# Kernel tuning notes

Hardware: AMD Instinct MI355X
Metric: run time of the kernel (lower is better)

Reference implementation:

```python
import jax, jax.numpy as jnp
import numpy as np

EPS = 1e-08   # clip eps from __init__
M = 0.2       # angular margin
B, D, C = 512, 512, 100000


def setup_inputs() -> dict:
    key = jax.random.key(0)
    k1, k2, k3 = jax.random.split(key, 3)
    x = jax.random.normal(k1, (B, D), dtype=jnp.float32)
    weight = jax.random.normal(k2, (C, D), dtype=jnp.float32)
    y = jax.random.randint(k3, (B,), 0, C, dtype=jnp.int64)
    rescale = jnp.ones((1,), dtype=jnp.float32)
    return {"x": x, "y": y, "weight": weight, "rescale": rescale}


def _l2norm(v, axis=-1, eps=1e-12):
    # matches F.normalize(p=2): v / max(||v||, eps)
    n = jnp.sqrt(jnp.sum(v * v, axis=axis, keepdims=True))
    return v / jnp.maximum(n, eps)


def reference(x, y, weight, rescale):
    # cos similarities: [B, C]
    fc = jnp.clip(_l2norm(x) @ _l2norm(weight).T, -1.0 + EPS, 1.0 - EPS)
    fc_w_margin = jnp.cos(jnp.arccos(fc) + M)
    # inject margin only at the target class (one-hot where-select)
    is_target = jax.nn.one_hot(y, C, dtype=jnp.bool_)
    logit = jnp.where(is_target, fc_w_margin, fc)
    # faithful to original: softmax, then CrossEntropyLoss on the probs
    res = jax.nn.softmax(rescale * logit, axis=-1)
    logp = jax.nn.log_softmax(res, axis=-1)
    nll = -jnp.take_along_axis(logp, y[:, None], axis=1)[:, 0]
    return jnp.mean(nll)
```

## Files before the change

### kernel.cpp

```cpp
#include <hip/hip_runtime.h>
#include <math.h>

#define BB 512
#define DD 512
#define CC 100000
#define CCPAD 100096
#define MARGIN 0.2f
#define CLIP_EPS 1e-8f
#define NCOLT 782

typedef float f32x4  __attribute__((ext_vector_type(4)));

#define XN8_BYTES   262144u
#define P_BYTES     1601536u
#define PBASE       XN8_BYTES
#define AUX_OFF     (PBASE + 3u * P_BYTES)

__device__ inline unsigned f2e4m3(float a) {
    unsigned u = __builtin_bit_cast(unsigned, a);
    unsigned s = (u >> 24) & 0x80u;
    float ab = fabsf(a);
    unsigned code;
    if (ab >= 0.015625f) {
        unsigned r = (u & 0x7FFFFFFFu) + 0x7FFFFu + ((u >> 20) & 1u);
        int e = (int)(r >> 23) - 127;
        unsigned m = (r >> 20) & 7u;
        code = (unsigned)((e + 7) << 3) | m;
    } else {
        code = (unsigned)rintf(ab * 512.0f);
    }
    return s | code;
}

__device__ inline int soff8(int row, int b) {
    return row * 64 + ((((b >> 4) ^ ((row >> 1) & 3)) << 4)) + (b & 15);
}

__global__ __launch_bounds__(256) void k_norm_x(const float* __restrict__ x,
                                                unsigned char* __restrict__ XN8,
                                                float* __restrict__ out) {
    int row = blockIdx.x, tid = threadIdx.x;
    float2 v = *(const float2*)(x + row * DD + tid * 2);
    float ss = v.x * v.x + v.y * v.y;
    for (int m = 1; m < 64; m <<= 1) ss += __shfl_xor(ss, m, 64);
    __shared__ float sm[4];
    int wid = tid >> 6, lane = tid & 63;
    if (lane == 0) sm[wid] = ss;
    __syncthreads();
    float inv = 1.0f / fmaxf(sqrtf(sm[0] + sm[1] + sm[2] + sm[3]), 1e-12f);
    unsigned c0 = f2e4m3(v.x * inv), c1 = f2e4m3(v.y * inv);
    *(unsigned short*)(XN8 + row * DD + tid * 2) = (unsigned short)(c0 | (c1 << 8));
    if (row == 0 && tid == 0) out[0] = 0.0f;
}

__global__ __launch_bounds__(256) void k_wnormc(const float* __restrict__ w,
                                                unsigned char* __restrict__ WN8) {
    int wid = threadIdx.x >> 6, lane = threadIdx.x & 63;
    int row = blockIdx.x * 4 + wid;
    unsigned* o0 = (unsigned*)(WN8 + (size_t)row * DD + 4 * lane);
    unsigned* o1 = (unsigned*)(WN8 + (size_t)row * DD + 256 + 4 * lane);
    if (row >= CC) { *o0 = 0u; *o1 = 0u; return; }
    const float4* wr = (const float4*)(w + (size_t)row * DD);
    float4 a = wr[lane];
    float4 b = wr[lane + 64];
    float ss = a.x*a.x + a.y*a.y + a.z*a.z + a.w*a.w
             + b.x*b.x + b.y*b.y + b.z*b.z + b.w*b.w;
    for (int m = 1; m < 64; m <<= 1) ss += __shfl_xor(ss, m, 64);
    float inv = 1.0f / fmaxf(sqrtf(ss), 1e-12f);
    *o0 = f2e4m3(a.x*inv) | (f2e4m3(a.y*inv) << 8) | (f2e4m3(a.z*inv) << 16) | (f2e4m3(a.w*inv) << 24);
    *o1 = f2e4m3(b.x*inv) | (f2e4m3(b.y*inv) << 8) | (f2e4m3(b.z*inv) << 16) | (f2e4m3(b.w*inv) << 24);
}

__global__ __launch_bounds__(256) void k_gemm8(const unsigned char* __restrict__ WN8,
                                               const unsigned char* __restrict__ XN8,
                                               const float* __restrict__ rescale_p,
                                               float* __restrict__ ZP,
                                               float* __restrict__ S2P,
                                               float* __restrict__ S3P) {
    __shared__ __align__(16) unsigned char Wt[3][128 * 64];
    __shared__ __align__(16) unsigned char Xs[3][128 * 64];
    __shared__ float st[2][2][64][3];

    int h = blockIdx.x;
    int logical = (h & 7) * 391 + (h >> 3);
    int ct = logical >> 2;
    int bt = logical & 3;

    int tid = threadIdx.x;
    int lane = tid & 63, wid = tid >> 6;
    int wr = wid >> 1, wc = wid & 1;
    float rescale = rescale_p[0];

    int rl0 = wid * 16 + (lane >> 2);
    int j0  = lane & 3;
    const unsigned char* wbase = WN8 + (size_t)(ct * 128) * DD;
    const unsigned char* xbase = XN8 + (size_t)(bt * 128) * DD;

    auto STAGE = [&](int b, int kt) {
#pragma unroll
        for (int i = 0; i < 2; ++i) {
            int rl = i * 64 + rl0;
            int jsrc = j0 ^ ((rl >> 1) & 3);
            const unsigned char* ws_ = wbase + (size_t)rl * DD + kt * 64 + jsrc * 16;
            const unsigned char* xs_ = xbase + (size_t)rl * DD + kt * 64 + jsrc * 16;
            unsigned char* wd = &Wt[b][(i * 256 + wid * 64) * 16];
            unsigned char* xd = &Xs[b][(i * 256 + wid * 64) * 16];
            __builtin_amdgcn_global_load_lds(
                (const __attribute__((address_space(1))) void*)ws_,
                (__attribute__((address_space(3))) void*)wd, 16, 0, 0);
            __builtin_amdgcn_global_load_lds(
                (const __attribute__((address_space(1))) void*)xs_,
                (__attribute__((address_space(3))) void*)xd, 16, 0, 0);
        }
    };

    int roA[2][4], roB[2][4];
#pragma unroll
    for (int sl = 0; sl < 2; ++sl)
#pragma unroll
        for (int i = 0; i < 4; ++i) {
            int bb = sl * 32 + (lane >> 4) * 8;
            roA[sl][i] = soff8(wr * 64 + i * 16 + (lane & 15), bb);
            roB[sl][i] = soff8(wc * 64 + i * 16 + (lane & 15), bb);
        }

    f32x4 acc[4][4];
#pragma unroll
    for (int i = 0; i < 4; i++)
#pragma unroll
        for (int j = 0; j < 4; j++) acc[i][j] = (f32x4){0.f, 0.f, 0.f, 0.f};

    auto COMPUTE = [&](int b) {
#pragma unroll
        for (int sl = 0; sl < 2; ++sl) {
            long a[4], bb[4];
#pragma unroll
            for (int i = 0; i < 4; i++) a[i]  = *(const long*)&Wt[b][roA[sl][i]];
#pragma unroll
            for (int i = 0; i < 4; i++) bb[i] = *(const long*)&Xs[b][roB[sl][i]];
#pragma unroll
            for (int i = 0; i < 4; i++)
#pragma unroll
                for (int j = 0; j < 4; j++)
                    acc[i][j] = __builtin_amdgcn_mfma_f32_16x16x32_fp8_fp8(a[i], bb[j], acc[i][j], 0, 0, 0);
        }
    };

    STAGE(0, 0);
    STAGE(1, 1);
    STAGE(2, 2);
    asm volatile("s_waitcnt vmcnt(8)" ::: "memory");
    __builtin_amdgcn_s_barrier();

    int cur = 0;
    for (int kt = 0; kt < 8; ++kt) {
        COMPUTE(cur);
        if (kt == 7) break;
        __builtin_amdgcn_s_barrier();
        if (kt < 5) {
            STAGE(cur, kt + 3);
            asm volatile("s_waitcnt vmcnt(8)" ::: "memory");
        } else if (kt == 5) {
            asm volatile("s_waitcnt vmcnt(4)" ::: "memory");
        } else {
            asm volatile("s_waitcnt vmcnt(0)" ::: "memory");
        }
        __builtin_amdgcn_s_barrier();
        cur = (cur == 2) ? 0 : cur + 1;
    }

    float mref = fabsf(rescale);
    const float L2E = 1.44269504f;
    float rs = rescale * L2E, mb = mref * L2E;
    float zz[4] = {0.f,0.f,0.f,0.f}, q2[4] = {0.f,0.f,0.f,0.f}, q3[4] = {0.f,0.f,0.f,0.f};
#pragma unroll
    for (int mi = 0; mi < 4; mi++) {
#pragma unroll
        for (int reg = 0; reg < 4; reg++) {
            int c = ct * 128 + wr * 64 + mi * 16 + (lane >> 4) * 4 + reg;
            float mask = (c < CC) ? 1.0f : 0.0f;
#pragma unroll
            for (int ni = 0; ni < 4; ni++) {
                float cosv = acc[mi][ni][reg];
                cosv = fminf(fmaxf(cosv, -1.0f + CLIP_EPS), 1.0f - CLIP_EPS);
                float e = exp2f(fmaf(cosv, rs, -mb)) * mask;
                float e2 = e * e;
                zz[ni] += e;
                q2[ni] += e2;
                q3[ni] = fmaf(e2, e, q3[ni]);
            }
        }
    }
#pragma unroll
    for (int msk = 16; msk < 64; msk <<= 1) {
#pragma unroll
        for (int ni = 0; ni < 4; ni++) {
            zz[ni] += __shfl_xor(zz[ni], msk, 64);
            q2[ni] += __shfl_xor(q2[ni], msk, 64);
            q3[ni] += __shfl_xor(q3[ni], msk, 64);
        }
    }
    if (lane < 16) {
#pragma unroll
        for (int ni = 0; ni < 4; ni++) {
            st[wc][wr][ni * 16 + lane][0] = zz[ni];
            st[wc][wr][ni * 16 + lane][1] = q2[ni];
            st[wc][wr][ni * 16 + lane][2] = q3[ni];
        }
    }
    __syncthreads();
    if (tid < 128) {
        int bh = tid >> 6, bl = tid & 63;
        float Z  = st[bh][0][bl][0] + st[bh][1][bl][0];
        float S2 = st[bh][0][bl][1] + st[bh][1][bl][1];
        float S3 = st[bh][0][bl][2] + st[bh][1][bl][2];
        size_t gi = (size_t)ct * BB + bt * 128 + tid;
        ZP[gi] = Z; S2P[gi] = S2; S3P[gi] = S3;
    }
}

__global__ __launch_bounds__(256) void k_final(const float* __restrict__ x,
                                               const float* __restrict__ w,
                                               const int* __restrict__ y,
                                               const float* __restrict__ rescale_p,
                                               const float* __restrict__ ZP,
                                               const float* __restrict__ S2P,
                                               const float* __restrict__ S3P,
                                               float* __restrict__ out) {
    int b = blockIdx.x, tid = threadIdx.x;
    int yb = y[b];

    float dq = 0.f, qx = 0.f, qw = 0.f;
#pragma unroll
    for (int i = 0; i < 2; i++) {
        int idx = tid + i * 256;
        float xv = x[b * DD + idx];
        float wv = w[(size_t)yb * DD + idx];
        dq = fmaf(xv, wv, dq);
        qx = fmaf(xv, xv, qx);
        qw = fmaf(wv, wv, qw);
    }
    for (int m = 1; m < 64; m <<= 1) {
        dq += __shfl_xor(dq, m, 64);
        qx += __shfl_xor(qx, m, 64);
        qw += __shfl_xor(qw, m, 64);
    }
    __shared__ float sd[4], sx[4], sw[4], szs[4], s2s[4], s3s[4];
    int wid = tid >> 6, lane = tid & 63;
    if (lane == 0) { sd[wid] = dq; sx[wid] = qx; sw[wid] = qw; }

    float rz = 0.f, r2 = 0.f, r3 = 0.f;
    for (int ch = tid; ch < NCOLT; ch += 256) {
        size_t gi = (size_t)ch * BB + b;
        rz += ZP[gi]; r2 += S2P[gi]; r3 += S3P[gi];
    }
    for (int m = 1; m < 64; m <<= 1) {
        rz += __shfl_xor(rz, m, 64);
        r2 += __shfl_xor(r2, m, 64);
        r3 += __shfl_xor(r3, m, 64);
    }
    if (lane == 0) { szs[wid] = rz; s2s[wid] = r2; s3s[wid] = r3; }
    __syncthreads();

    if (tid == 0) {
        float Z  = szs[0] + szs[1] + szs[2] + szs[3];
        float S2 = s2s[0] + s2s[1] + s2s[2] + s2s[3];
        float S3 = s3s[0] + s3s[1] + s3s[2] + s3s[3];
        float dot = sd[0] + sd[1] + sd[2] + sd[3];
        float ssx = sx[0] + sx[1] + sx[2] + sx[3];
        float ssw = sw[0] + sw[1] + sw[2] + sw[3];
        float rescale = rescale_p[0];
        float mref = fabsf(rescale);
        float fc = dot / (fmaxf(sqrtf(ssx), 1e-12f) * fmaxf(sqrtf(ssw), 1e-12f));
        fc = fminf(fmaxf(fc, -1.0f + CLIP_EPS), 1.0f - CLIP_EPS);
        float su = rescale * fc;
        float fcm = fc * cosf(MARGIN) - sqrtf(fmaxf(1.0f - fc * fc, 0.0f)) * sinf(MARGIN);
        float smv = rescale * fcm;
        float eU = __expf(su - mref), eM = __expf(smv - mref);
        Z  += eM - eU;
        S2 += eM * eM - eU * eU;
        S3 += eM * eM * eM - eU * eU * eU;
        float py = eM / Z;
        float sumexp = (float)CC + 1.0f + S2 / (2.0f * Z * Z) + S3 / (6.0f * Z * Z * Z);
        float nll = logf(sumexp) - py;
        atomicAdd(out, nll * (1.0f / (float)BB));
    }
}

extern "C" void kernel_launch(void* const* d_in, const int* in_sizes, int n_in,
                              void* d_out, int out_size, void* d_ws, size_t ws_size,
                              hipStream_t stream) {
    const float* x       = (const float*)d_in[0];
    const int*   y       = (const int*)  d_in[1];
    const float* w       = (const float*)d_in[2];
    const float* rescale = (const float*)d_in[3];
    float* out = (float*)d_out;
    char*  wsb = (char*)d_ws;

    unsigned char* XN8 = (unsigned char*)(wsb);
    float* ZP  = (float*)(wsb + PBASE);
    float* S2P = (float*)(wsb + PBASE + P_BYTES);
    float* S3P = (float*)(wsb + PBASE + 2u * P_BYTES);
    unsigned char* WN8 = (unsigned char*)(wsb + AUX_OFF);

    k_norm_x<<<dim3(BB), dim3(256), 0, stream>>>(x, XN8, out);
    k_wnormc<<<dim3(CCPAD / 4), dim3(256), 0, stream>>>(w, WN8);
    k_gemm8 <<<dim3(8 * 391), dim3(256), 0, stream>>>(WN8, XN8, rescale, ZP, S2P, S3P);
    k_final <<<dim3(BB), dim3(256), 0, stream>>>(x, w, y, rescale, ZP, S2P, S3P, out);
}
```

Baseline: 112.0 us.

## Fuse weight normalization and fp8 quantization into the GEMM mainloop

Drops the separate weight normalize/quantize pass that wrote and re-read an fp8 copy of W. The GEMM now streams fp32 W rows into registers, accumulates the squared norms and converts them to fp8 in LDS. It applies the inverse norm to the accumulators in the epilogue. Tiles are retiled so each 512-thread block handles 64 classes against all 512 batch rows, which removes the repeated W tile reads across batch tiles. In exchange the blocks need much more LDS and quantize unnormalized values, which shifts the fp8 rounding behaviour.

Result: slower. 147.9 us (+32.0%).

```diff
diff --git a/kernel.cpp b/kernel.cpp
--- a/kernel.cpp
+++ b/kernel.cpp
@@ -4,17 +4,15 @@
 #define BB 512
 #define DD 512
 #define CC 100000
-#define CCPAD 100096
 #define MARGIN 0.2f
 #define CLIP_EPS 1e-8f
-#define NCOLT 782
+#define NCT 1563
 
 typedef float f32x4  __attribute__((ext_vector_type(4)));
 
 #define XN8_BYTES   262144u
-#define P_BYTES     1601536u
+#define P_BYTES     3201024u
 #define PBASE       XN8_BYTES
-#define AUX_OFF     (PBASE + 3u * P_BYTES)
 
 __device__ inline unsigned f2e4m3(float a) {
     unsigned u = __builtin_bit_cast(unsigned, a);
@@ -53,135 +51,141 @@
     if (row == 0 && tid == 0) out[0] = 0.0f;
 }
 
-__global__ __launch_bounds__(256) void k_wnormc(const float* __restrict__ w,
-                                                unsigned char* __restrict__ WN8) {
-    int wid = threadIdx.x >> 6, lane = threadIdx.x & 63;
-    int row = blockIdx.x * 4 + wid;
-    unsigned* o0 = (unsigned*)(WN8 + (size_t)row * DD + 4 * lane);
-    unsigned* o1 = (unsigned*)(WN8 + (size_t)row * DD + 256 + 4 * lane);
-    if (row >= CC) { *o0 = 0u; *o1 = 0u; return; }
-    const float4* wr = (const float4*)(w + (size_t)row * DD);
-    float4 a = wr[lane];
-    float4 b = wr[lane + 64];
-    float ss = a.x*a.x + a.y*a.y + a.z*a.z + a.w*a.w
-             + b.x*b.x + b.y*b.y + b.z*b.z + b.w*b.w;
-    for (int m = 1; m < 64; m <<= 1) ss += __shfl_xor(ss, m, 64);
-    float inv = 1.0f / fmaxf(sqrtf(ss), 1e-12f);
-    *o0 = f2e4m3(a.x*inv) | (f2e4m3(a.y*inv) << 8) | (f2e4m3(a.z*inv) << 16) | (f2e4m3(a.w*inv) << 24);
-    *o1 = f2e4m3(b.x*inv) | (f2e4m3(b.y*inv) << 8) | (f2e4m3(b.z*inv) << 16) | (f2e4m3(b.w*inv) << 24);
-}
-
-__global__ __launch_bounds__(256) void k_gemm8(const unsigned char* __restrict__ WN8,
-                                               const unsigned char* __restrict__ XN8,
-                                               const float* __restrict__ rescale_p,
-                                               float* __restrict__ ZP,
-                                               float* __restrict__ S2P,
-                                               float* __restrict__ S3P) {
-    __shared__ __align__(16) unsigned char Wt[3][128 * 64];
-    __shared__ __align__(16) unsigned char Xs[3][128 * 64];
-    __shared__ float st[2][2][64][3];
-
-    int h = blockIdx.x;
-    int logical = (h & 7) * 391 + (h >> 3);
-    int ct = logical >> 2;
-    int bt = logical & 3;
-
+__global__ __launch_bounds__(512, 2) void k_gemmf(const float* __restrict__ w,
+                                                  const unsigned char* __restrict__ XN8,
+                                                  const float* __restrict__ rescale_p,
+                                                  float* __restrict__ ZP,
+                                                  float* __restrict__ S2P,
+                                                  float* __restrict__ S3P) {
+    __shared__ __align__(16) unsigned char Xs[3][512 * 64];
+    __shared__ __align__(16) unsigned char Wt[3][64 * 64];
+    __shared__ float wsum[64];
+
+    int ct = blockIdx.x;
     int tid = threadIdx.x;
     int lane = tid & 63, wid = tid >> 6;
-    int wr = wid >> 1, wc = wid & 1;
+    int cgr = wid >> 2;
+    int bgr = wid & 3;
     float rescale = rescale_p[0];
 
-    int rl0 = wid * 16 + (lane >> 2);
-    int j0  = lane & 3;
-    const unsigned char* wbase = WN8 + (size_t)(ct * 128) * DD;
-    const unsigned char* xbase = XN8 + (size_t)(bt * 128) * DD;
-
-    auto STAGE = [&](int b, int kt) {
-#pragma unroll
-        for (int i = 0; i < 2; ++i) {
-            int rl = i * 64 + rl0;
-            int jsrc = j0 ^ ((rl >> 1) & 3);
-            const unsigned char* ws_ = wbase + (size_t)rl * DD + kt * 64 + jsrc * 16;
-            const unsigned char* xs_ = xbase + (size_t)rl * DD + kt * 64 + jsrc * 16;
-            unsigned char* wd = &Wt[b][(i * 256 + wid * 64) * 16];
-            unsigned char* xd = &Xs[b][(i * 256 + wid * 64) * 16];
+    int wrl = tid >> 3, wsub = tid & 7;
+    int cg = ct * 64 + wrl;
+    int cgc = cg < CC ? cg : CC - 1;
+    const float4* wsrc = (const float4*)(w + (size_t)cgc * DD);
+
+    const unsigned char* xbase = XN8;
+    auto STAGE_X = [&](int buf, int kt) {
+#pragma unroll
+        for (int i = 0; i < 4; ++i) {
+            int ch = i * 512 + tid;
+            int rl = ch >> 2;
+            int jsrc = (ch & 3) ^ ((rl >> 1) & 3);
+            const unsigned char* src = xbase + (size_t)rl * DD + kt * 64 + jsrc * 16;
+            unsigned char* dst = &Xs[buf][(i * 512 + wid * 64) * 16];
             __builtin_amdgcn_global_load_lds(
-                (const __attribute__((address_space(1))) void*)ws_,
-                (__attribute__((address_space(3))) void*)wd, 16, 0, 0);
-            __builtin_amdgcn_global_load_lds(
-                (const __attribute__((address_space(1))) void*)xs_,
-                (__attribute__((address_space(3))) void*)xd, 16, 0, 0);
+                (const __attribute__((address_space(1))) void*)src,
+                (__attribute__((address_space(3))) void*)dst, 16, 0, 0);
         }
     };
 
-    int roA[2][4], roB[2][4];
-#pragma unroll
-    for (int sl = 0; sl < 2; ++sl)
-#pragma unroll
-        for (int i = 0; i < 4; ++i) {
-            int bb = sl * 32 + (lane >> 4) * 8;
-            roA[sl][i] = soff8(wr * 64 + i * 16 + (lane & 15), bb);
-            roB[sl][i] = soff8(wc * 64 + i * 16 + (lane & 15), bb);
-        }
-
-    f32x4 acc[4][4];
-#pragma unroll
-    for (int i = 0; i < 4; i++)
-#pragma unroll
-        for (int j = 0; j < 4; j++) acc[i][j] = (f32x4){0.f, 0.f, 0.f, 0.f};
-
-    auto COMPUTE = [&](int b) {
+    float4 wrg[3][2];
+    float swacc = 0.f;
+    auto LOAD_W = [&](int slot, int kt) {
+        wrg[slot][0] = wsrc[kt * 16 + wsub * 2];
+        wrg[slot][1] = wsrc[kt * 16 + wsub * 2 + 1];
+    };
+    auto CONV_W = [&](int slot, int buf) {
+        float4 a = wrg[slot][0], b = wrg[slot][1];
+        swacc += a.x*a.x + a.y*a.y + a.z*a.z + a.w*a.w
+               + b.x*b.x + b.y*b.y + b.z*b.z + b.w*b.w;
+        unsigned lo = f2e4m3(a.x) | (f2e4m3(a.y) << 8) | (f2e4m3(a.z) << 16) | (f2e4m3(a.w) << 24);
+        unsigned hi = f2e4m3(b.x) | (f2e4m3(b.y) << 8) | (f2e4m3(b.z) << 16) | (f2e4m3(b.w) << 24);
+        *(uint2*)&Wt[buf][soff8(wrl, wsub * 8)] = make_uint2(lo, hi);
+    };
+
+    int roA[2][2], roB[2][8];
+#pragma unroll
+    for (int sl = 0; sl < 2; ++sl) {
+        int kb = sl * 32 + (lane >> 4) * 8;
+#pragma unroll
+        for (int mi = 0; mi < 2; ++mi)
+            roA[sl][mi] = soff8(cgr * 32 + mi * 16 + (lane & 15), kb);
+#pragma unroll
+        for (int ni = 0; ni < 8; ++ni)
+            roB[sl][ni] = soff8(bgr * 128 + ni * 16 + (lane & 15), kb);
+    }
+
+    f32x4 acc[2][8];
+#pragma unroll
+    for (int i = 0; i < 2; i++)
+#pragma unroll
+        for (int j = 0; j < 8; j++) acc[i][j] = (f32x4){0.f, 0.f, 0.f, 0.f};
+
+    auto COMPUTE = [&](int buf) {
 #pragma unroll
         for (int sl = 0; sl < 2; ++sl) {
-            long a[4], bb[4];
-#pragma unroll
-            for (int i = 0; i < 4; i++) a[i]  = *(const long*)&Wt[b][roA[sl][i]];
-#pragma unroll
-            for (int i = 0; i < 4; i++) bb[i] = *(const long*)&Xs[b][roB[sl][i]];
-#pragma unroll
-            for (int i = 0; i < 4; i++)
-#pragma unroll
-                for (int j = 0; j < 4; j++)
+            long a[2], bb[8];
+#pragma unroll
+            for (int i = 0; i < 2; i++) a[i]  = *(const long*)&Wt[buf][roA[sl][i]];
+#pragma unroll
+            for (int i = 0; i < 8; i++) bb[i] = *(const long*)&Xs[buf][roB[sl][i]];
+#pragma unroll
+            for (int i = 0; i < 2; i++)
+#pragma unroll
+                for (int j = 0; j < 8; j++)
                     acc[i][j] = __builtin_amdgcn_mfma_f32_16x16x32_fp8_fp8(a[i], bb[j], acc[i][j], 0, 0, 0);
         }
     };
 
-    STAGE(0, 0);
-    STAGE(1, 1);
-    STAGE(2, 2);
+    LOAD_W(0, 0);
+    STAGE_X(0, 0);
+    LOAD_W(1, 1);
+    STAGE_X(1, 1);
+    LOAD_W(2, 2);
     asm volatile("s_waitcnt vmcnt(8)" ::: "memory");
+    CONV_W(0, 0);
+    asm volatile("s_waitcnt lgkmcnt(0)" ::: "memory");
     __builtin_amdgcn_s_barrier();
 
-    int cur = 0;
+#pragma unroll
     for (int kt = 0; kt < 8; ++kt) {
-        COMPUTE(cur);
-        if (kt == 7) break;
-        __builtin_amdgcn_s_barrier();
-        if (kt < 5) {
-            STAGE(cur, kt + 3);
-            asm volatile("s_waitcnt vmcnt(8)" ::: "memory");
-        } else if (kt == 5) {
-            asm volatile("s_waitcnt vmcnt(4)" ::: "memory");
-        } else {
-            asm volatile("s_waitcnt vmcnt(0)" ::: "memory");
-        }
-        __builtin_amdgcn_s_barrier();
-        cur = (cur == 2) ? 0 : cur + 1;
-    }
-
+        if (kt + 2 <= 7) STAGE_X((kt + 2) % 3, kt + 2);
+        if (kt + 3 <= 7) LOAD_W((kt + 3) % 3, kt + 3);
+        if (kt <= 4)      { asm volatile("s_waitcnt vmcnt(8)" ::: "memory"); }
+        else if (kt == 5) { asm volatile("s_waitcnt vmcnt(6)" ::: "memory"); }
+        else if (kt == 6) { asm volatile("s_waitcnt vmcnt(0)" ::: "memory"); }
+        if (kt + 1 <= 7) CONV_W((kt + 1) % 3, (kt + 1) % 3);
+        COMPUTE(kt % 3);
+        if (kt < 7) {
+            asm volatile("s_waitcnt lgkmcnt(0)" ::: "memory");
+            __builtin_amdgcn_s_barrier();
+        }
+    }
+
+    __syncthreads();
+#pragma unroll
+    for (int m = 1; m < 8; m <<= 1) swacc += __shfl_xor(swacc, m, 64);
+    if (wsub == 0) wsum[wrl] = swacc;
+    __syncthreads();
+
+    float* stp = (float*)&Xs[0][0];
     float mref = fabsf(rescale);
     const float L2E = 1.44269504f;
     float rs = rescale * L2E, mb = mref * L2E;
-    float zz[4] = {0.f,0.f,0.f,0.f}, q2[4] = {0.f,0.f,0.f,0.f}, q3[4] = {0.f,0.f,0.f,0.f};
-#pragma unroll
-    for (int mi = 0; mi < 4; mi++) {
+    float zz[8], q2[8], q3[8];
+#pragma unroll
+    for (int ni = 0; ni < 8; ni++) { zz[ni] = 0.f; q2[ni] = 0.f; q3[ni] = 0.f; }
+#pragma unroll
+    for (int mi = 0; mi < 2; mi++) {
 #pragma unroll
         for (int reg = 0; reg < 4; reg++) {
-            int c = ct * 128 + wr * 64 + mi * 16 + (lane >> 4) * 4 + reg;
+            int cl = cgr * 32 + mi * 16 + (lane >> 4) * 4 + reg;
+            int c  = ct * 64 + cl;
             float mask = (c < CC) ? 1.0f : 0.0f;
-#pragma unroll
-            for (int ni = 0; ni < 4; ni++) {
-                float cosv = acc[mi][ni][reg];
+            float winv = 1.0f / fmaxf(sqrtf(wsum[cl]), 1e-12f);
+#pragma unroll
+            for (int ni = 0; ni < 8; ni++) {
+                float cosv = acc[mi][ni][reg] * winv;
                 cosv = fminf(fmaxf(cosv, -1.0f + CLIP_EPS), 1.0f - CLIP_EPS);
                 float e = exp2f(fmaf(cosv, rs, -mb)) * mask;
                 float e2 = e * e;
@@ -194,7 +198,7 @@
 #pragma unroll
     for (int msk = 16; msk < 64; msk <<= 1) {
 #pragma unroll
-        for (int ni = 0; ni < 4; ni++) {
+        for (int ni = 0; ni < 8; ni++) {
             zz[ni] += __shfl_xor(zz[ni], msk, 64);
             q2[ni] += __shfl_xor(q2[ni], msk, 64);
             q3[ni] += __shfl_xor(q3[ni], msk, 64);
@@ -202,19 +206,19 @@
     }
     if (lane < 16) {
 #pragma unroll
-        for (int ni = 0; ni < 4; ni++) {
-            st[wc][wr][ni * 16 + lane][0] = zz[ni];
-            st[wc][wr][ni * 16 + lane][1] = q2[ni];
-            st[wc][wr][ni * 16 + lane][2] = q3[ni];
-        }
-    }
-    __syncthreads();
-    if (tid < 128) {
-        int bh = tid >> 6, bl = tid & 63;
-        float Z  = st[bh][0][bl][0] + st[bh][1][bl][0];
-        float S2 = st[bh][0][bl][1] + st[bh][1][bl][1];
-        float S3 = st[bh][0][bl][2] + st[bh][1][bl][2];
-        size_t gi = (size_t)ct * BB + bt * 128 + tid;
+        for (int ni = 0; ni < 8; ni++) {
+            int col = bgr * 128 + ni * 16 + lane;
+            stp[(cgr * 512 + col) * 3 + 0] = zz[ni];
+            stp[(cgr * 512 + col) * 3 + 1] = q2[ni];
+            stp[(cgr * 512 + col) * 3 + 2] = q3[ni];
+        }
+    }
+    __syncthreads();
+    {
+        float Z  = stp[(0 * 512 + tid) * 3 + 0] + stp[(1 * 512 + tid) * 3 + 0];
+        float S2 = stp[(0 * 512 + tid) * 3 + 1] + stp[(1 * 512 + tid) * 3 + 1];
+        float S3 = stp[(0 * 512 + tid) * 3 + 2] + stp[(1 * 512 + tid) * 3 + 2];
+        size_t gi = (size_t)ct * BB + tid;
         ZP[gi] = Z; S2P[gi] = S2; S3P[gi] = S3;
     }
 }
@@ -250,7 +254,7 @@
     if (lane == 0) { sd[wid] = dq; sx[wid] = qx; sw[wid] = qw; }
 
     float rz = 0.f, r2 = 0.f, r3 = 0.f;
-    for (int ch = tid; ch < NCOLT; ch += 256) {
+    for (int ch = tid; ch < NCT; ch += 256) {
         size_t gi = (size_t)ch * BB + b;
         rz += ZP[gi]; r2 += S2P[gi]; r3 += S3P[gi];
     }
@@ -301,10 +305,8 @@
     float* ZP  = (float*)(wsb + PBASE);
     float* S2P = (float*)(wsb + PBASE + P_BYTES);
     float* S3P = (float*)(wsb + PBASE + 2u * P_BYTES);
-    unsigned char* WN8 = (unsigned char*)(wsb + AUX_OFF);
 
     k_norm_x<<<dim3(BB), dim3(256), 0, stream>>>(x, XN8, out);
-    k_wnormc<<<dim3(CCPAD / 4), dim3(256), 0, stream>>>(w, WN8);
-    k_gemm8 <<<dim3(8 * 391), dim3(256), 0, stream>>>(WN8, XN8, rescale, ZP, S2P, S3P);
+    k_gemmf <<<dim3(NCT), dim3(512), 0, stream>>>(w, XN8, rescale, ZP, S2P, S3P);
     k_final <<<dim3(BB), dim3(256), 0, stream>>>(x, w, y, rescale, ZP, S2P, S3P, out);
 }
```

## Merge x/W normalization kernels and permute K layout for 128-bit LDS reads

Applied to the files above, without the earlier changes.

Replaces the two normalization kernels with one prep kernel that handles both W and x rows, which drops a launch. The kernel also writes the fp8 data with a K-permuted layout, so the GEMM can read 16 bytes per LDS load and run two MFMA passes on the halves. This halves the number of LDS read instructions in the inner loop. The permutation must be identical for both operands for the dot products to stay correct. The prep kernel's global writes change from 4-byte to 8-byte stores, but its reads become less contiguous.

New measurement: 105.6 us, median of 2. -5.7%, faster.

```diff
diff --git a/kernel.cpp b/kernel.cpp
--- a/kernel.cpp
+++ b/kernel.cpp
@@ -10,6 +10,7 @@
 #define NCOLT 782
 
 typedef float f32x4  __attribute__((ext_vector_type(4)));
+typedef long  lx2    __attribute__((ext_vector_type(2)));
 
 #define XN8_BYTES   262144u
 #define P_BYTES     1601536u
@@ -36,39 +37,39 @@
     return row * 64 + ((((b >> 4) ^ ((row >> 1) & 3)) << 4)) + (b & 15);
 }
 
-__global__ __launch_bounds__(256) void k_norm_x(const float* __restrict__ x,
-                                                unsigned char* __restrict__ XN8,
-                                                float* __restrict__ out) {
-    int row = blockIdx.x, tid = threadIdx.x;
-    float2 v = *(const float2*)(x + row * DD + tid * 2);
-    float ss = v.x * v.x + v.y * v.y;
-    for (int m = 1; m < 64; m <<= 1) ss += __shfl_xor(ss, m, 64);
-    __shared__ float sm[4];
-    int wid = tid >> 6, lane = tid & 63;
-    if (lane == 0) sm[wid] = ss;
-    __syncthreads();
-    float inv = 1.0f / fmaxf(sqrtf(sm[0] + sm[1] + sm[2] + sm[3]), 1e-12f);
-    unsigned c0 = f2e4m3(v.x * inv), c1 = f2e4m3(v.y * inv);
-    *(unsigned short*)(XN8 + row * DD + tid * 2) = (unsigned short)(c0 | (c1 << 8));
-    if (row == 0 && tid == 0) out[0] = 0.0f;
-}
-
-__global__ __launch_bounds__(256) void k_wnormc(const float* __restrict__ w,
-                                                unsigned char* __restrict__ WN8) {
-    int wid = threadIdx.x >> 6, lane = threadIdx.x & 63;
-    int row = blockIdx.x * 4 + wid;
-    unsigned* o0 = (unsigned*)(WN8 + (size_t)row * DD + 4 * lane);
-    unsigned* o1 = (unsigned*)(WN8 + (size_t)row * DD + 256 + 4 * lane);
-    if (row >= CC) { *o0 = 0u; *o1 = 0u; return; }
-    const float4* wr = (const float4*)(w + (size_t)row * DD);
-    float4 a = wr[lane];
-    float4 b = wr[lane + 64];
+
+__global__ __launch_bounds__(256) void k_prep(const float* __restrict__ w,
+                                              const float* __restrict__ x,
+                                              unsigned char* __restrict__ WN8,
+                                              unsigned char* __restrict__ XN8,
+                                              float* __restrict__ out) {
+    int wv = threadIdx.x >> 6, lane = threadIdx.x & 63;
+    int r = blockIdx.x * 4 + wv;
+    const float* src;
+    unsigned char* dst;
+    bool zero = false;
+    if (r < CCPAD) {
+        zero = (r >= CC);
+        src = w + (size_t)(zero ? 0 : r) * DD;
+        dst = WN8 + (size_t)r * DD;
+    } else {
+        int xr = r - CCPAD;
+        src = x + (size_t)xr * DD;
+        dst = XN8 + (size_t)xr * DD;
+    }
+    int o  = lane * 8;
+    int K0 = (o & ~63) + ((o >> 3) & 1) * 32 + ((o >> 4) & 3) * 8;
+    float4 a = *(const float4*)(src + K0);
+    float4 b = *(const float4*)(src + K0 + 4);
+    if (zero) { a = make_float4(0.f,0.f,0.f,0.f); b = a; }
     float ss = a.x*a.x + a.y*a.y + a.z*a.z + a.w*a.w
              + b.x*b.x + b.y*b.y + b.z*b.z + b.w*b.w;
     for (int m = 1; m < 64; m <<= 1) ss += __shfl_xor(ss, m, 64);
     float inv = 1.0f / fmaxf(sqrtf(ss), 1e-12f);
-    *o0 = f2e4m3(a.x*inv) | (f2e4m3(a.y*inv) << 8) | (f2e4m3(a.z*inv) << 16) | (f2e4m3(a.w*inv) << 24);
-    *o1 = f2e4m3(b.x*inv) | (f2e4m3(b.y*inv) << 8) | (f2e4m3(b.z*inv) << 16) | (f2e4m3(b.w*inv) << 24);
+    unsigned lo = f2e4m3(a.x*inv) | (f2e4m3(a.y*inv) << 8) | (f2e4m3(a.z*inv) << 16) | (f2e4m3(a.w*inv) << 24);
+    unsigned hi = f2e4m3(b.x*inv) | (f2e4m3(b.y*inv) << 8) | (f2e4m3(b.z*inv) << 16) | (f2e4m3(b.w*inv) << 24);
+    *(uint2*)(dst + o) = make_uint2(lo, hi);
+    if (blockIdx.x == 0 && threadIdx.x == 0) out[0] = 0.0f;
 }
 
 __global__ __launch_bounds__(256) void k_gemm8(const unsigned char* __restrict__ WN8,
@@ -114,15 +115,13 @@
         }
     };
 
-    int roA[2][4], roB[2][4];
-#pragma unroll
-    for (int sl = 0; sl < 2; ++sl)
-#pragma unroll
-        for (int i = 0; i < 4; ++i) {
-            int bb = sl * 32 + (lane >> 4) * 8;
-            roA[sl][i] = soff8(wr * 64 + i * 16 + (lane & 15), bb);
-            roB[sl][i] = soff8(wc * 64 + i * 16 + (lane & 15), bb);
-        }
+    int roA[4], roB[4];
+#pragma unroll
+    for (int i = 0; i < 4; ++i) {
+        int kb = (lane >> 4) * 16;
+        roA[i] = soff8(wr * 64 + i * 16 + (lane & 15), kb);
+        roB[i] = soff8(wc * 64 + i * 16 + (lane & 15), kb);
+    }
 
     f32x4 acc[4][4];
 #pragma unroll
@@ -131,19 +130,21 @@
         for (int j = 0; j < 4; j++) acc[i][j] = (f32x4){0.f, 0.f, 0.f, 0.f};
 
     auto COMPUTE = [&](int b) {
-#pragma unroll
-        for (int sl = 0; sl < 2; ++sl) {
-            long a[4], bb[4];
-#pragma unroll
-            for (int i = 0; i < 4; i++) a[i]  = *(const long*)&Wt[b][roA[sl][i]];
-#pragma unroll
-            for (int i = 0; i < 4; i++) bb[i] = *(const long*)&Xs[b][roB[sl][i]];
-#pragma unroll
-            for (int i = 0; i < 4; i++)
-#pragma unroll
-                for (int j = 0; j < 4; j++)
-                    acc[i][j] = __builtin_amdgcn_mfma_f32_16x16x32_fp8_fp8(a[i], bb[j], acc[i][j], 0, 0, 0);
-        }
+        lx2 a[4], bb[4];
+#pragma unroll
+        for (int i = 0; i < 4; i++) a[i]  = *(const lx2*)&Wt[b][roA[i]];
+#pragma unroll
+        for (int i = 0; i < 4; i++) bb[i] = *(const lx2*)&Xs[b][roB[i]];
+#pragma unroll
+        for (int i = 0; i < 4; i++)
+#pragma unroll
+            for (int j = 0; j < 4; j++)
+                acc[i][j] = __builtin_amdgcn_mfma_f32_16x16x32_fp8_fp8(a[i][0], bb[j][0], acc[i][j], 0, 0, 0);
+#pragma unroll
+        for (int i = 0; i < 4; i++)
+#pragma unroll
+            for (int j = 0; j < 4; j++)
+                acc[i][j] = __builtin_amdgcn_mfma_f32_16x16x32_fp8_fp8(a[i][1], bb[j][1], acc[i][j], 0, 0, 0);
     };
 
     STAGE(0, 0);
@@ -303,8 +304,7 @@
     float* S3P = (float*)(wsb + PBASE + 2u * P_BYTES);
     unsigned char* WN8 = (unsigned char*)(wsb + AUX_OFF);
 
-    k_norm_x<<<dim3(BB), dim3(256), 0, stream>>>(x, XN8, out);
-    k_wnormc<<<dim3(CCPAD / 4), dim3(256), 0, stream>>>(w, WN8);
+    k_prep  <<<dim3(CCPAD / 4 + BB / 4), dim3(256), 0, stream>>>(w, x, WN8, XN8, out);
     k_gemm8 <<<dim3(8 * 391), dim3(256), 0, stream>>>(WN8, XN8, rescale, ZP, S2P, S3P);
     k_final <<<dim3(BB), dim3(256), 0, stream>>>(x, w, y, rescale, ZP, S2P, S3P, out);
 }
```
